# Kernel optimization log

Measured on AMD Instinct MI355X. Metric: run time of the kernel, lower is better.

## Reference

```python
import jax, jax.numpy as jnp
import numpy as np

EPS = 1e-07
ORTH_LAMBDA = 0.1
KAMA = 1.0


def setup_inputs() -> dict:
    key = jax.random.key(0)
    ks = jax.random.split(key, 10)
    b, c, h, w, n = 8, 128, 128, 128, 16
    s = 0.05  # weight init scale
    return {
        "x":     jax.random.normal(ks[0], (b, c, h, w), jnp.float32),
        "Wsa":   jax.random.normal(ks[1], (c, c), jnp.float32) * s,
        "bsa":   jnp.zeros((c,), jnp.float32),
        "Wr":    jax.random.normal(ks[2], (c, c), jnp.float32) * s,
        "br":    jnp.zeros((c,), jnp.float32),
        "kn":    jax.random.normal(ks[3], (n, c), jnp.float32),  # (nClass, in_c, 1, 1) squeezed
        "Wo":    jax.random.normal(ks[4], (c, c), jnp.float32) * s,
        "bo":    jnp.zeros((c,), jnp.float32),
        "alpha": jnp.ones((1, n, 1), jnp.float32) * 0.1,
        "sigma": jnp.ones((1,), jnp.float32) * 0.5,  # torch inits 0; nonzero so out != x
    }


def reference(x, Wsa, bsa, Wr, br, kn, Wo, bo, alpha, sigma):
    b, c, h, w = x.shape
    n = kn.shape[0]
    hw = h * w

    conv1x1 = lambda W, bb: jnp.einsum('oc,bchw->bohw', W, x) + bb[:, None, None]
    xsa = conv1x1(Wsa, bsa)                       # (b,c,h,w)
    xr = conv1x1(Wr, br)                          # (b,c,h,w)
    xo = conv1x1(Wo, bo)                          # (b,c,h,w)
    xn = jnp.einsum('nc,bchw->bnhw', kn, x)       # (b,n,h,w), no bias

    # ---- orthogonality loss over class kernels ----
    sym = kn @ kn.T                               # (n,n)
    nrm = jnp.sqrt(jnp.sum(kn ** 2, axis=-1, keepdims=True))  # (n,1)
    loss = sym / (nrm @ nrm.T + EPS) - jnp.eye(n, dtype=x.dtype)
    orth_loss = ORTH_LAMBDA * jnp.log(jnp.sum(loss ** 2) + 1.0)

    xsa_r = xsa.reshape(b, c, hw)
    xr_r = xr.reshape(b, c, hw)
    xn_r = xn.reshape(b, n, hw)

    # ---- cosine-normalized class-channel relation ----
    relation = jnp.einsum('bnk,bck->bnc', xn_r, xr_r)            # (b,n,c)
    norm_xr = jnp.sqrt(jnp.sum(xr_r ** 2, axis=-1, keepdims=True))  # (b,c,1)
    norm_xn = jnp.sqrt(jnp.sum(xn_r ** 2, axis=-1, keepdims=True))  # (b,n,1)
    relation_norm = relation / (norm_xn @ jnp.swapaxes(norm_xr, 1, 2) + EPS)

    # ---- channel self-attention regularizer ----
    rela = jnp.einsum('bik,bjk->bij', xsa_r, xsa_r)              # (b,c,c)
    factor = rela * (1.0 - jnp.eye(c, dtype=x.dtype))
    regular = jax.nn.softmax(jnp.mean(factor, axis=1, keepdims=True), axis=-1)  # (b,1,c)

    alpha_c = jnp.clip(alpha, 0.0, 1.0)                          # (1,n,1)
    relation_norm = (relation_norm + alpha_c * regular) / KAMA
    att = jax.nn.softmax(relation_norm, axis=1)                  # (b,n,c)

    # ---- fused attention-weighted group norm (no (b,n,c,h,w) materialization)
    # hot_area[b,n,c,h,w] = xo[b,c,h,w] * att[b,n,c]; reductions over (c,h,w)
    s1 = jnp.sum(xo, axis=(2, 3))                                # (b,c) sum_hw xo
    s2 = jnp.sum(xo ** 2, axis=(2, 3))                           # (b,c) sum_hw xo^2
    cnt = jnp.sum(att, axis=2) * hw + EPS                        # (b,n)
    hot_sum = jnp.einsum('bnc,bc->bn', att, s1)                  # (b,n)
    fo_mean = hot_sum / cnt                                      # (b,n)
    sq = jnp.einsum('bnc,bc->bn', att ** 2, s2) - 2.0 * fo_mean * hot_sum \
         + (fo_mean ** 2) * (c * hw)
    fo_std = jnp.sqrt(sq / cnt)                                  # (b,n)

    # out[b,c,h,w] = sum_n (xo - mean)/(std+eps) * att = xo*A - B
    inv = 1.0 / (fo_std + EPS)                                   # (b,n)
    A = jnp.einsum('bnc,bn->bc', att, inv)                       # (b,c)
    B = jnp.einsum('bnc,bn->bc', att, fo_mean * inv)             # (b,c)
    out = x + sigma * (xo * A[:, :, None, None] - B[:, :, None, None])
    return out, orth_loss
```

## Files before the change

### kernel.cpp

```cpp
#include <hip/hip_runtime.h>
#include <hip/hip_bf16.h>

#define B_   8
#define C_   128
#define HW_  16384
#define N_   16
#define EPS_ 1e-7f

typedef unsigned short u16;
typedef __attribute__((ext_vector_type(8))) short s8v;
typedef __attribute__((ext_vector_type(4))) short s4v;
typedef __attribute__((ext_vector_type(4))) float f4v;

__device__ __forceinline__ u16 f2b(float f) {
  union { __hip_bfloat16 b; u16 u; } cv; cv.b = __float2bfloat16(f); return cv.u;
}
__device__ __forceinline__ float b2f(u16 u) {
  union { float f; unsigned int i; } cv; cv.i = ((unsigned int)u) << 16; return cv.f;
}
__device__ __forceinline__ float wredsum(float v) {
#pragma unroll
  for (int o = 32; o > 0; o >>= 1) v += __shfl_xor(v, o, 64);
  return v;
}
__device__ __forceinline__ float wredmax(float v) {
#pragma unroll
  for (int o = 32; o > 0; o >>= 1) v = fmaxf(v, __shfl_xor(v, o, 64));
  return v;
}

#define XS_ 136
__global__ __launch_bounds__(256, 2) void k_gram(const float* __restrict__ x,
                                                 float* __restrict__ G,
                                                 float* __restrict__ sx) {
  const int b  = blockIdx.y;
  const int p0 = blockIdx.x * 256;
  __shared__ u16 Xb[C_ * XS_];
  const int tid = threadIdx.x;
  const int lane = tid & 63;
  const int w = tid >> 6;
  const int m = lane & 15, q = lane >> 4;
  const int rb = (w >> 1) * 64, cb = (w & 1) * 64;

  f4v acc[4][4];
#pragma unroll
  for (int a = 0; a < 4; ++a)
#pragma unroll
    for (int c2 = 0; c2 < 4; ++c2) acc[a][c2] = (f4v){0.f, 0.f, 0.f, 0.f};

  float sxp = 0.f;
  const float* xb = x + (size_t)b * C_ * HW_;

  for (int t = 0; t < 2; ++t) {
#pragma unroll
    for (int j = 0; j < 16; ++j) {
      int flat = tid + 256 * j;
      int c = flat >> 5, qf = flat & 31;
      float4 v = *(const float4*)(xb + (size_t)c * HW_ + p0 + t * 128 + 4 * qf);
      s4v s; s[0] = (short)f2b(v.x); s[1] = (short)f2b(v.y);
      s[2] = (short)f2b(v.z); s[3] = (short)f2b(v.w);
      *(s4v*)(&Xb[c * XS_ + 4 * qf]) = s;
    }
    __syncthreads();
    if (tid < C_) {
#pragma unroll
      for (int kk = 0; kk < 16; ++kk) {
        s8v vv = *(const s8v*)(&Xb[tid * XS_ + 8 * kk]);
#pragma unroll
        for (int e = 0; e < 8; ++e) sxp += b2f((u16)vv[e]);
      }
    }
#pragma unroll
    for (int s = 0; s < 4; ++s) {
      const int k0 = 32 * s;
      s8v Af[4], Bf[4];
#pragma unroll
      for (int a = 0; a < 4; ++a)
        Af[a] = *(const s8v*)(&Xb[(rb + 16 * a + m) * XS_ + k0 + 8 * q]);
#pragma unroll
      for (int c2 = 0; c2 < 4; ++c2)
        Bf[c2] = *(const s8v*)(&Xb[(cb + 16 * c2 + m) * XS_ + k0 + 8 * q]);
#pragma unroll
      for (int a = 0; a < 4; ++a)
#pragma unroll
        for (int c2 = 0; c2 < 4; ++c2)
          acc[a][c2] = __builtin_amdgcn_mfma_f32_16x16x32_bf16(Af[a], Bf[c2], acc[a][c2], 0, 0, 0);
    }
    __syncthreads();
  }

  float* Gb = G + b * C_ * C_;
#pragma unroll
  for (int a = 0; a < 4; ++a)
#pragma unroll
    for (int c2 = 0; c2 < 4; ++c2)
#pragma unroll
      for (int r = 0; r < 4; ++r) {
        int row = rb + 16 * a + 4 * q + r;
        int col = cb + 16 * c2 + m;
        atomicAdd(&Gb[row * C_ + col], acc[a][c2][r]);
      }
  if (tid < C_) atomicAdd(&sx[b * C_ + tid], sxp);
}

__global__ void k_u(const float* __restrict__ Wsa, float* __restrict__ u) {
  int r = threadIdx.x;
  float s = 0.f;
  for (int i = 0; i < C_; ++i) s += Wsa[i * C_ + r];
  u[r] = s;
}

__global__ __launch_bounds__(64) void k_cols(
    const float* __restrict__ G, const float* __restrict__ sx,
    const float* __restrict__ Wr, const float* __restrict__ Wsa,
    const float* __restrict__ Wo, const float* __restrict__ kn,
    const float* __restrict__ u,
    float* diagR, float* diagSA, float* colsumSA, float* diagO,
    float* prv, float* psav, float* pov, float* rel, float* diagN, float* ksx) {
  const int b = blockIdx.y;
  const int col = blockIdx.x;
  const int lane = threadIdx.x;
  const float* Gb = G + b * C_ * C_;
  const float4* g0 = (const float4*)(Gb + lane * C_);
  const float4* g1 = (const float4*)(Gb + (64 + lane) * C_);
  const float sx0 = sx[b * C_ + lane], sx1 = sx[b * C_ + 64 + lane];

  if (col < C_) {
    const float4* wr = (const float4*)(Wr + col * C_);
    const float4* wa = (const float4*)(Wsa + col * C_);
    const float4* wo = (const float4*)(Wo + col * C_);
    float t0r = 0, t1r = 0, t0a = 0, t1a = 0, t0o = 0, t1o = 0;
    for (int c = 0; c < 32; ++c) {
      float4 a0 = g0[c], a1 = g1[c];
      float4 vr = wr[c], va = wa[c], vo = wo[c];
      t0r += a0.x * vr.x + a0.y * vr.y + a0.z * vr.z + a0.w * vr.w;
      t1r += a1.x * vr.x + a1.y * vr.y + a1.z * vr.z + a1.w * vr.w;
      t0a += a0.x * va.x + a0.y * va.y + a0.z * va.z + a0.w * va.w;
      t1a += a1.x * va.x + a1.y * va.y + a1.z * va.z + a1.w * va.w;
      t0o += a0.x * vo.x + a0.y * vo.y + a0.z * vo.z + a0.w * vo.w;
      t1o += a1.x * vo.x + a1.y * vo.y + a1.z * vo.z + a1.w * vo.w;
    }
    float wr0 = Wr[col * C_ + lane], wr1 = Wr[col * C_ + 64 + lane];
    float wa0 = Wsa[col * C_ + lane], wa1 = Wsa[col * C_ + 64 + lane];
    float wo0 = Wo[col * C_ + lane], wo1 = Wo[col * C_ + 64 + lane];
    float u0 = u[lane], u1 = u[64 + lane];
    float dR = wredsum(wr0 * t0r + wr1 * t1r);
    float pR = wredsum(wr0 * sx0 + wr1 * sx1);
    float dA = wredsum(wa0 * t0a + wa1 * t1a);
    float cA = wredsum(u0 * t0a + u1 * t1a);
    float pA = wredsum(wa0 * sx0 + wa1 * sx1);
    float dO = wredsum(wo0 * t0o + wo1 * t1o);
    float pO = wredsum(wo0 * sx0 + wo1 * sx1);
    float rl[N_];
#pragma unroll
    for (int n = 0; n < N_; ++n)
      rl[n] = wredsum(kn[n * C_ + lane] * t0r + kn[n * C_ + 64 + lane] * t1r);
    if (lane == 0) {
      diagR[b * C_ + col] = dR;  prv[b * C_ + col] = pR;
      diagSA[b * C_ + col] = dA; colsumSA[b * C_ + col] = cA; psav[b * C_ + col] = pA;
      diagO[b * C_ + col] = dO;  pov[b * C_ + col] = pO;
      for (int n = 0; n < N_; ++n) rel[(b * N_ + n) * C_ + col] = rl[n];
    }
  } else {
    const int n = col - C_;
    const float4* wk = (const float4*)(kn + n * C_);
    float t0 = 0, t1 = 0;
    for (int c = 0; c < 32; ++c) {
      float4 a0 = g0[c], a1 = g1[c], vk = wk[c];
      t0 += a0.x * vk.x + a0.y * vk.y + a0.z * vk.z + a0.w * vk.w;
      t1 += a1.x * vk.x + a1.y * vk.y + a1.z * vk.z + a1.w * vk.w;
    }
    float k0v = kn[n * C_ + lane], k1v = kn[n * C_ + 64 + lane];
    float dN = wredsum(k0v * t0 + k1v * t1);
    float kx = wredsum(k0v * sx0 + k1v * sx1);
    if (lane == 0) { diagN[b * N_ + n] = dN; ksx[b * N_ + n] = kx; }
  }
}

__global__ __launch_bounds__(128) void k_asm(
    const float* diagR, const float* diagSA, const float* colsumSA, const float* diagO,
    const float* prv, const float* psav, const float* pov,
    const float* rel, const float* diagN, const float* ksx,
    const float* br, const float* bo, const float* bsa, const float* alpha,
    float* Aout, float* Bout) {
  const int b = blockIdx.x;
  const int t = threadIdx.x;
  __shared__ float rb2[2];
  __shared__ float att_s[N_][C_ + 1];
  __shared__ float s1_s[C_], s2_s[C_];
  __shared__ float inv_s[N_], fmi_s[N_];
  const float hw = (float)HW_;
  const float bsa_c = bsa[t], br_c = br[t], bo_c = bo[t];
  const float psa_c = psav[b * C_ + t], pr_c = prv[b * C_ + t], po_c = pov[b * C_ + t];

  float bsum, psum, mx, ssum;
  { float wv = wredsum(bsa_c); if ((t & 63) == 0) rb2[t >> 6] = wv; __syncthreads();
    bsum = rb2[0] + rb2[1]; __syncthreads(); }
  { float wv = wredsum(psa_c); if ((t & 63) == 0) rb2[t >> 6] = wv; __syncthreads();
    psum = rb2[0] + rb2[1]; __syncthreads(); }

  const float nxr = sqrtf(fmaxf(diagR[b * C_ + t] + 2.f * br_c * pr_c + hw * br_c * br_c, 0.f));
  s1_s[t] = po_c + hw * bo_c;
  s2_s[t] = diagO[b * C_ + t] + 2.f * bo_c * po_c + hw * bo_c * bo_c;
  const float colsum = colsumSA[b * C_ + t] + bsum * psa_c + bsa_c * (psum + hw * bsum);
  const float diagv = diagSA[b * C_ + t] + 2.f * bsa_c * psa_c + hw * bsa_c * bsa_c;
  const float fm = (colsum - diagv) * (1.f / (float)C_);

  { float wv = wredmax(fm); if ((t & 63) == 0) rb2[t >> 6] = wv; __syncthreads();
    mx = fmaxf(rb2[0], rb2[1]); __syncthreads(); }
  const float ee = expf(fm - mx);
  { float wv = wredsum(ee); if ((t & 63) == 0) rb2[t >> 6] = wv; __syncthreads();
    ssum = rb2[0] + rb2[1]; __syncthreads(); }
  const float reg = ee / ssum;

  float r[N_];
  float rmax = -1e30f;
#pragma unroll
  for (int n = 0; n < N_; ++n) {
    float al = fminf(fmaxf(alpha[n], 0.f), 1.f);
    float nxn = sqrtf(fmaxf(diagN[b * N_ + n], 0.f));
    float rv = (rel[(b * N_ + n) * C_ + t] + br_c * ksx[b * N_ + n]) / (nxn * nxr + EPS_) + al * reg;
    r[n] = rv; rmax = fmaxf(rmax, rv);
  }
  float es = 0.f;
#pragma unroll
  for (int n = 0; n < N_; ++n) { r[n] = expf(r[n] - rmax); es += r[n]; }
  const float ies = 1.f / es;
#pragma unroll
  for (int n = 0; n < N_; ++n) att_s[n][t] = r[n] * ies;
  __syncthreads();

  if (t < N_) {
    float sa = 0.f, sh = 0.f, sq = 0.f;
    for (int c = 0; c < C_; ++c) {
      float a = att_s[t][c];
      sa += a; sh += a * s1_s[c]; sq += a * a * s2_s[c];
    }
    float cnt = sa * hw + EPS_;
    float fmean = sh / cnt;
    float sqv = sq - 2.f * fmean * sh + fmean * fmean * ((float)C_ * hw);
    float fstd = sqrtf(fmaxf(sqv, 0.f) / cnt);
    float inv = 1.f / (fstd + EPS_);
    inv_s[t] = inv; fmi_s[t] = fmean * inv;
  }
  __syncthreads();

  float Ac = 0.f, Bc = 0.f;
#pragma unroll
  for (int n = 0; n < N_; ++n) { float a = att_s[n][t]; Ac += a * inv_s[n]; Bc += a * fmi_s[n]; }
  Aout[b * C_ + t] = Ac; Bout[b * C_ + t] = Bc;
}

__global__ __launch_bounds__(256) void k_orth(const float* __restrict__ kn,
                                              float* __restrict__ out_loss) {
  const int t = threadIdx.x;
  const int i = t >> 4, j = t & 15;
  float s = 0.f;
  for (int c = 0; c < C_; ++c) s += kn[i * C_ + c] * kn[j * C_ + c];
  __shared__ float nrm[N_];
  __shared__ float rb4[4];
  if (i == j) nrm[i] = sqrtf(s);
  __syncthreads();
  float l = s / (nrm[i] * nrm[j] + EPS_) - (i == j ? 1.f : 0.f);
  float wv = wredsum(l * l);
  if ((t & 63) == 0) rb4[t >> 6] = wv;
  __syncthreads();
  if (t == 0) out_loss[0] = 0.1f * logf(rb4[0] + rb4[1] + rb4[2] + rb4[3] + 1.f);
}

#define WS2_ 136
#define XS2_ 68
__global__ __launch_bounds__(256, 2) void k_out(
    const float* __restrict__ x, const float* __restrict__ Wo,
    const float* __restrict__ bo, const float* __restrict__ Aws,
    const float* __restrict__ Bws, const float* __restrict__ sig,
    float* __restrict__ out) {
  const int b = blockIdx.y;
  const int chunk = blockIdx.x;
  __shared__ u16 Wob[C_ * WS2_];
  __shared__ u16 Xb[C_ * XS2_];
  __shared__ float As[C_], Bs[C_], bos[C_];
  const int tid = threadIdx.x, lane = tid & 63, w = tid >> 6;
  const int n = lane & 15, q = lane >> 4;

#pragma unroll
  for (int j = 0; j < 16; ++j) {
    int flat = tid + 256 * j;
    int o = flat >> 5, qf = flat & 31;
    float4 v = *(const float4*)(Wo + o * C_ + 4 * qf);
    s4v s; s[0] = (short)f2b(v.x); s[1] = (short)f2b(v.y);
    s[2] = (short)f2b(v.z); s[3] = (short)f2b(v.w);
    *(s4v*)(&Wob[o * WS2_ + 4 * qf]) = s;
  }
  if (tid < C_) { As[tid] = Aws[b * C_ + tid]; Bs[tid] = Bws[b * C_ + tid]; bos[tid] = bo[tid]; }
  const float sg = sig[0];
  __syncthreads();

  const float* xb = x + (size_t)b * C_ * HW_;
  float* ob = out + (size_t)b * C_ * HW_;

  for (int pt = 0; pt < 8; ++pt) {
    const int p0 = chunk * 512 + pt * 64;
#pragma unroll
    for (int j = 0; j < 8; ++j) {
      int flat = tid + 256 * j;
      int c = flat >> 4, qf = flat & 15;
      float4 v = *(const float4*)(xb + (size_t)c * HW_ + p0 + 4 * qf);
      s4v s; s[0] = (short)f2b(v.x); s[1] = (short)f2b(v.y);
      s[2] = (short)f2b(v.z); s[3] = (short)f2b(v.w);
      *(s4v*)(&Xb[c * XS2_ + 4 * qf]) = s;
    }
    __syncthreads();

    f4v acc[8];
#pragma unroll
    for (int a = 0; a < 8; ++a) acc[a] = (f4v){0.f, 0.f, 0.f, 0.f};
#pragma unroll
    for (int s = 0; s < 4; ++s) {
      const int k0 = 32 * s;
      union { s8v v; u16 u[8]; } bfr;
#pragma unroll
      for (int i = 0; i < 8; ++i)
        bfr.u[i] = Xb[(k0 + 8 * q + i) * XS2_ + w * 16 + n];
#pragma unroll
      for (int a = 0; a < 8; ++a) {
        s8v af = *(const s8v*)(&Wob[(16 * a + n) * WS2_ + k0 + 8 * q]);
        acc[a] = __builtin_amdgcn_mfma_f32_16x16x32_bf16(af, bfr.v, acc[a], 0, 0, 0);
      }
    }
    __syncthreads();

#pragma unroll
    for (int a = 0; a < 8; ++a)
#pragma unroll
      for (int r = 0; r < 4; ++r) {
        int o = 16 * a + 4 * q + r;
        size_t idx = (size_t)o * HW_ + p0 + w * 16 + n;
        float xo = acc[a][r] + bos[o];
        ob[idx] = xb[idx] + sg * (xo * As[o] - Bs[o]);
      }
  }
}

extern "C" void kernel_launch(void* const* d_in, const int* in_sizes, int n_in,
                              void* d_out, int out_size, void* d_ws, size_t ws_size,
                              hipStream_t stream) {
  (void)in_sizes; (void)n_in; (void)out_size; (void)ws_size;
  const float* x     = (const float*)d_in[0];
  const float* Wsa   = (const float*)d_in[1];
  const float* bsa   = (const float*)d_in[2];
  const float* Wr    = (const float*)d_in[3];
  const float* br    = (const float*)d_in[4];
  const float* kn    = (const float*)d_in[5];
  const float* Wo    = (const float*)d_in[6];
  const float* bo    = (const float*)d_in[7];
  const float* alpha = (const float*)d_in[8];
  const float* sigma = (const float*)d_in[9];
  float* out = (float*)d_out;
  float* ws  = (float*)d_ws;

  float* G        = ws;
  float* sx       = ws + 131072;
  float* diagR    = ws + 132096;
  float* diagSA   = ws + 133120;
  float* colsumSA = ws + 134144;
  float* diagO    = ws + 135168;
  float* prv      = ws + 136192;
  float* psav     = ws + 137216;
  float* pov      = ws + 138240;
  float* rel      = ws + 139264;
  float* diagN    = ws + 155648;
  float* ksx      = ws + 155776;
  float* u        = ws + 155904;
  float* Aw       = ws + 156032;
  float* Bw       = ws + 157056;

  hipMemsetAsync(G, 0, (131072 + 1024) * sizeof(float), stream);
  k_gram<<<dim3(64, 8), 256, 0, stream>>>(x, G, sx);
  k_u<<<1, 128, 0, stream>>>(Wsa, u);
  k_cols<<<dim3(144, 8), 64, 0, stream>>>(G, sx, Wr, Wsa, Wo, kn, u,
      diagR, diagSA, colsumSA, diagO, prv, psav, pov, rel, diagN, ksx);
  k_asm<<<8, 128, 0, stream>>>(diagR, diagSA, colsumSA, diagO, prv, psav, pov,
      rel, diagN, ksx, br, bo, bsa, alpha, Aw, Bw);
  k_orth<<<1, 256, 0, stream>>>(kn, out + (size_t)B_ * C_ * HW_);
  k_out<<<dim3(32, 8), 256, 0, stream>>>(x, Wo, bo, Aw, Bw, sigma, out);
}
```

Measured before the change: 220.7 us.

## Replace Gram atomics with partial buffers and reduction, transpose X tile in k_out

The Gram kernel now writes per-block partial 128x128 results into a scratch area (the output buffer, reused before k_out runs) instead of issuing global atomicAdds, and a new reduction kernel sums the 64 partials. This removes atomic contention and the memset, at the cost of writing and reading about 32 MB of partials. k_out now stages X transposed in shared memory so the MFMA B-fragment is a single vector LDS load rather than 8 scalar loads. It also doubles the grid, halves the work per block and raises occupancy hints.

```diff
diff --git a/kernel.cpp b/kernel.cpp
--- a/kernel.cpp
+++ b/kernel.cpp
@@ -30,9 +30,9 @@
 }
 
 #define XS_ 136
-__global__ __launch_bounds__(256, 2) void k_gram(const float* __restrict__ x,
-                                                 float* __restrict__ G,
-                                                 float* __restrict__ sx) {
+__global__ __launch_bounds__(256, 4) void k_gram(const float* __restrict__ x,
+                                                 float* __restrict__ pbuf,
+                                                 float* __restrict__ psx) {
   const int b  = blockIdx.y;
   const int p0 = blockIdx.x * 256;
   __shared__ u16 Xb[C_ * XS_];
@@ -89,7 +89,7 @@
     __syncthreads();
   }
 
-  float* Gb = G + b * C_ * C_;
+  float* pg = pbuf + ((size_t)(blockIdx.x * B_ + b) << 14);
 #pragma unroll
   for (int a = 0; a < 4; ++a)
 #pragma unroll
@@ -98,9 +98,30 @@
       for (int r = 0; r < 4; ++r) {
         int row = rb + 16 * a + 4 * q + r;
         int col = cb + 16 * c2 + m;
-        atomicAdd(&Gb[row * C_ + col], acc[a][c2][r]);
+        pg[row * C_ + col] = acc[a][c2][r];
       }
-  if (tid < C_) atomicAdd(&sx[b * C_ + tid], sxp);
+  if (tid < C_) psx[(blockIdx.x * B_ + b) * C_ + tid] = sxp;
+}
+
+__global__ __launch_bounds__(256) void k_greduce(const float* __restrict__ pbuf,
+                                                 const float* __restrict__ psx,
+                                                 float* __restrict__ G,
+                                                 float* __restrict__ sx) {
+  const int t = blockIdx.x * 256 + threadIdx.x;
+  if (blockIdx.x < 512) {
+    const int b = t >> 14, idx = t & 16383;
+    float s = 0.f;
+#pragma unroll 8
+    for (int ch = 0; ch < 64; ++ch) s += pbuf[((size_t)(ch * B_ + b) << 14) + idx];
+    G[t] = s;
+  } else {
+    const int tt = t - 131072;
+    const int b = tt >> 7, c = tt & 127;
+    float s = 0.f;
+#pragma unroll 8
+    for (int ch = 0; ch < 64; ++ch) s += psx[(ch * B_ + b) * C_ + c];
+    sx[tt] = s;
+  }
 }
 
 __global__ void k_u(const float* __restrict__ Wsa, float* __restrict__ u) {
@@ -268,17 +289,16 @@
   if (t == 0) out_loss[0] = 0.1f * logf(rb4[0] + rb4[1] + rb4[2] + rb4[3] + 1.f);
 }
 
-#define WS2_ 136
-#define XS2_ 68
-__global__ __launch_bounds__(256, 2) void k_out(
+#define WS2_ 132
+#define XT_  132
+__global__ __launch_bounds__(256, 3) void k_out(
     const float* __restrict__ x, const float* __restrict__ Wo,
     const float* __restrict__ bo, const float* __restrict__ Aws,
     const float* __restrict__ Bws, const float* __restrict__ sig,
     float* __restrict__ out) {
   const int b = blockIdx.y;
-  const int chunk = blockIdx.x;
   __shared__ u16 Wob[C_ * WS2_];
-  __shared__ u16 Xb[C_ * XS2_];
+  __shared__ u16 Xt[64 * XT_];
   __shared__ float As[C_], Bs[C_], bos[C_];
   const int tid = threadIdx.x, lane = tid & 63, w = tid >> 6;
   const int n = lane & 15, q = lane >> 4;
@@ -299,16 +319,26 @@
   const float* xb = x + (size_t)b * C_ * HW_;
   float* ob = out + (size_t)b * C_ * HW_;
 
-  for (int pt = 0; pt < 8; ++pt) {
-    const int p0 = chunk * 512 + pt * 64;
-#pragma unroll
-    for (int j = 0; j < 8; ++j) {
-      int flat = tid + 256 * j;
-      int c = flat >> 4, qf = flat & 15;
-      float4 v = *(const float4*)(xb + (size_t)c * HW_ + p0 + 4 * qf);
-      s4v s; s[0] = (short)f2b(v.x); s[1] = (short)f2b(v.y);
-      s[2] = (short)f2b(v.z); s[3] = (short)f2b(v.w);
-      *(s4v*)(&Xb[c * XS2_ + 4 * qf]) = s;
+  for (int pt = 0; pt < 4; ++pt) {
+    const int p0 = blockIdx.x * 256 + pt * 64;
+#pragma unroll
+    for (int cc = 0; cc < 2; ++cc) {
+      int cell = cc * 256 + tid;
+      int pq = cell & 15, c4 = cell >> 4;
+      const float* src = xb + (size_t)(4 * c4) * HW_ + p0 + 4 * pq;
+      float4 v0 = *(const float4*)(src);
+      float4 v1 = *(const float4*)(src + HW_);
+      float4 v2 = *(const float4*)(src + 2 * HW_);
+      float4 v3 = *(const float4*)(src + 3 * HW_);
+      s4v s0, s1, s2, s3;
+      s0[0] = (short)f2b(v0.x); s0[1] = (short)f2b(v1.x); s0[2] = (short)f2b(v2.x); s0[3] = (short)f2b(v3.x);
+      s1[0] = (short)f2b(v0.y); s1[1] = (short)f2b(v1.y); s1[2] = (short)f2b(v2.y); s1[3] = (short)f2b(v3.y);
+      s2[0] = (short)f2b(v0.z); s2[1] = (short)f2b(v1.z); s2[2] = (short)f2b(v2.z); s2[3] = (short)f2b(v3.z);
+      s3[0] = (short)f2b(v0.w); s3[1] = (short)f2b(v1.w); s3[2] = (short)f2b(v2.w); s3[3] = (short)f2b(v3.w);
+      *(s4v*)(&Xt[(4 * pq + 0) * XT_ + 4 * c4]) = s0;
+      *(s4v*)(&Xt[(4 * pq + 1) * XT_ + 4 * c4]) = s1;
+      *(s4v*)(&Xt[(4 * pq + 2) * XT_ + 4 * c4]) = s2;
+      *(s4v*)(&Xt[(4 * pq + 3) * XT_ + 4 * c4]) = s3;
     }
     __syncthreads();
 
@@ -318,14 +348,11 @@
 #pragma unroll
     for (int s = 0; s < 4; ++s) {
       const int k0 = 32 * s;
-      union { s8v v; u16 u[8]; } bfr;
-#pragma unroll
-      for (int i = 0; i < 8; ++i)
-        bfr.u[i] = Xb[(k0 + 8 * q + i) * XS2_ + w * 16 + n];
+      s8v bfr = *(const s8v*)(&Xt[(w * 16 + n) * XT_ + k0 + 8 * q]);
 #pragma unroll
       for (int a = 0; a < 8; ++a) {
         s8v af = *(const s8v*)(&Wob[(16 * a + n) * WS2_ + k0 + 8 * q]);
-        acc[a] = __builtin_amdgcn_mfma_f32_16x16x32_bf16(af, bfr.v, acc[a], 0, 0, 0);
+        acc[a] = __builtin_amdgcn_mfma_f32_16x16x32_bf16(af, bfr, acc[a], 0, 0, 0);
       }
     }
     __syncthreads();
@@ -375,13 +402,16 @@
   float* Aw       = ws + 156032;
   float* Bw       = ws + 157056;
 
-  hipMemsetAsync(G, 0, (131072 + 1024) * sizeof(float), stream);
-  k_gram<<<dim3(64, 8), 256, 0, stream>>>(x, G, sx);
+  float* pbuf = out;
+  float* psx  = out + 8388608;
+
+  k_gram<<<dim3(64, 8), 256, 0, stream>>>(x, pbuf, psx);
+  k_greduce<<<516, 256, 0, stream>>>(pbuf, psx, G, sx);
   k_u<<<1, 128, 0, stream>>>(Wsa, u);
   k_cols<<<dim3(144, 8), 64, 0, stream>>>(G, sx, Wr, Wsa, Wo, kn, u,
       diagR, diagSA, colsumSA, diagO, prv, psav, pov, rel, diagN, ksx);
   k_asm<<<8, 128, 0, stream>>>(diagR, diagSA, colsumSA, diagO, prv, psav, pov,
       rel, diagN, ksx, br, bo, bsa, alpha, Aw, Bw);
   k_orth<<<1, 256, 0, stream>>>(kn, out + (size_t)B_ * C_ * HW_);
-  k_out<<<dim3(32, 8), 256, 0, stream>>>(x, Wo, bo, Aw, Bw, sigma, out);
-}
+  k_out<<<dim3(64, 8), 256, 0, stream>>>(x, Wo, bo, Aw, Bw, sigma, out);
+}
```

Result: no change. 216.7 us (-1.8%).
